# Optimization experiments

Hardware: AMD Instinct MI355X
Metric: run time of the kernel (lower is better)

The kernel has to match this reference:

```python
import jax, jax.numpy as jnp
import numpy as np

EMBED = 768
HEAD = 128

def setup_inputs() -> dict:
    key = jax.random.key(0)
    ks = jax.random.split(key, 8)
    B, S = 8, 2048
    x = jax.random.normal(ks[0], (B, S, EMBED), dtype=jnp.float32)
    enc_output = jax.random.normal(ks[1], (B, S, EMBED), dtype=jnp.float32)
    s = 1.0 / np.sqrt(EMBED)
    Wq = jax.random.normal(ks[2], (EMBED, HEAD), dtype=jnp.float32) * s
    Wk = jax.random.normal(ks[3], (EMBED, HEAD), dtype=jnp.float32) * s
    Wv = jax.random.normal(ks[4], (EMBED, HEAD), dtype=jnp.float32) * s
    bq = jnp.zeros((HEAD,), dtype=jnp.float32)
    bk = jnp.zeros((HEAD,), dtype=jnp.float32)
    bv = jnp.zeros((HEAD,), dtype=jnp.float32)
    return {"x": x, "enc_output": enc_output, "Wq": Wq, "bq": bq,
            "Wk": Wk, "bk": bk, "Wv": Wv, "bv": bv}

def reference(x, enc_output, Wq, bq, Wk, bk, Wv, bv):
    # Faithful to original: Q, K, V all from x (enc_output is unused in the
    # original forward); scale is embed_size ** 0.5; dropout never applied.
    q = jnp.einsum('nse,ed->nsd', x, Wq) + bq  # [B,S,H]
    k = jnp.einsum('nse,ed->nsd', x, Wk) + bk
    v = jnp.einsum('nse,ed->nsd', x, Wv) + bv
    energy = jnp.einsum('nqd,nkd->nqk', q, k)  # [B,S,S]
    attn = jax.nn.softmax(energy / jnp.sqrt(jnp.float32(EMBED)), axis=2)
    out = jnp.einsum('nql,nld->nqd', attn, v)  # [B,S,H]
    return out
```

## Files before the change

### kernel.cpp

```cpp
#include <hip/hip_runtime.h>
#include <hip/hip_bf16.h>


typedef __bf16 bf16x8 __attribute__((ext_vector_type(8)));
typedef float f32x4 __attribute__((ext_vector_type(4)));
using bf16 = __hip_bfloat16;

#define EMB 768
#define HD 128
#define SEQ 2048
#define BATCH 8
#define ROWS (BATCH * SEQ)
#define NSPLIT 4
#define TILES_PER_SPLIT (SEQ / 64 / NSPLIT)

__device__ inline void cvt_store8(bf16* dst, float4 a, float4 b) {
    union { bf16 h[8]; uint4 u; } t;
    t.h[0] = __float2bfloat16(a.x); t.h[1] = __float2bfloat16(a.y);
    t.h[2] = __float2bfloat16(a.z); t.h[3] = __float2bfloat16(a.w);
    t.h[4] = __float2bfloat16(b.x); t.h[5] = __float2bfloat16(b.y);
    t.h[6] = __float2bfloat16(b.z); t.h[7] = __float2bfloat16(b.w);
    *reinterpret_cast<uint4*>(dst) = t.u;
}

__global__ __launch_bounds__(256) void wt_kernel(
    const float* __restrict__ Wq, const float* __restrict__ Wk,
    const float* __restrict__ Wv, bf16* __restrict__ Wt)
{
    __shared__ float t_lds[32][33];
    const int tid = threadIdx.x;
    const int k0 = blockIdx.x * 32;
    const int n0 = blockIdx.y * 32;
    const int mtx = blockIdx.z;
    const float* W = (mtx == 0) ? Wq : (mtx == 1) ? Wk : Wv;
    const int j = tid & 31, i0 = tid >> 5;
#pragma unroll
    for (int c = 0; c < 4; ++c)
        t_lds[i0 + 8 * c][j] = W[(size_t)(k0 + i0 + 8 * c) * HD + n0 + j];
    __syncthreads();
#pragma unroll
    for (int c = 0; c < 4; ++c)
        Wt[(size_t)mtx * HD * EMB + (size_t)(n0 + i0 + 8 * c) * EMB + k0 + j] =
            __float2bfloat16(t_lds[j][i0 + 8 * c]);
}

__global__ __launch_bounds__(256) void qkv_kernel(
    const float* __restrict__ x, const bf16* __restrict__ Wt,
    const float* __restrict__ bq, const float* __restrict__ bk,
    const float* __restrict__ bv,
    bf16* __restrict__ Q, bf16* __restrict__ K, bf16* __restrict__ Vt)
{
    __shared__ alignas(16) bf16 a_lds[64][68];
    __shared__ alignas(16) bf16 b_lds[128][68];
    const int tid  = threadIdx.x;
    const int sel  = blockIdx.y;
    const int row0 = blockIdx.x * 64;
    const bf16* Wsel = Wt + (size_t)sel * HD * EMB;
    const int lane = tid & 63, wave = tid >> 6;
    const int lr = lane & 15, lq = lane >> 4;

    f32x4 acc[8];
#pragma unroll
    for (int j = 0; j < 8; ++j) acc[j] = f32x4{0.f, 0.f, 0.f, 0.f};

    for (int kt = 0; kt < EMB / 64; ++kt) {
#pragma unroll
        for (int c = 0; c < 2; ++c) {
            int lin = tid + c * 256;
            int r = lin >> 3, ch = lin & 7;
            const float* src = &x[(size_t)(row0 + r) * EMB + kt * 64 + ch * 8];
            float4 f0 = *reinterpret_cast<const float4*>(src);
            float4 f1 = *reinterpret_cast<const float4*>(src + 4);
            cvt_store8(&a_lds[r][ch * 8], f0, f1);
        }
#pragma unroll
        for (int c = 0; c < 4; ++c) {
            int lin = tid + c * 256;
            int r = lin >> 3, ch = lin & 7;
            *reinterpret_cast<uint4*>(&b_lds[r][ch * 8]) =
                *reinterpret_cast<const uint4*>(&Wsel[(size_t)r * EMB + kt * 64 + ch * 8]);
        }
        __syncthreads();
#pragma unroll
        for (int ks = 0; ks < 2; ++ks) {
            bf16x8 a = *reinterpret_cast<const bf16x8*>(&a_lds[wave * 16 + lr][ks * 32 + lq * 8]);
#pragma unroll
            for (int nt = 0; nt < 8; ++nt) {
                bf16x8 b = *reinterpret_cast<const bf16x8*>(&b_lds[nt * 16 + lr][ks * 32 + lq * 8]);
                acc[nt] = __builtin_amdgcn_mfma_f32_16x16x32_bf16(a, b, acc[nt], 0, 0, 0);
            }
        }
        __syncthreads();
    }

    bf16 (*o_lds)[132] = reinterpret_cast<bf16(*)[132]>(&b_lds[0][0]);
    const float* bias = (sel == 0) ? bq : (sel == 1) ? bk : bv;
#pragma unroll
    for (int nt = 0; nt < 8; ++nt) {
        int col = nt * 16 + lr;
        float bb = bias[col];
#pragma unroll
        for (int rg = 0; rg < 4; ++rg)
            o_lds[wave * 16 + lq * 4 + rg][col] = __float2bfloat16(acc[nt][rg] + bb);
    }
    __syncthreads();
    if (sel < 2) {
        bf16* dst = (sel == 0) ? Q : K;
#pragma unroll
        for (int c = 0; c < 4; ++c) {
            int lin = tid + c * 256;
            int r = lin >> 4, ch = lin & 15;
            *reinterpret_cast<uint4*>(&dst[(size_t)(row0 + r) * HD + ch * 8]) =
                *reinterpret_cast<const uint4*>(&o_lds[r][ch * 8]);
        }
    } else {
        int d = tid >> 1, sh = (tid & 1) * 32;
        int bi = row0 >> 11, s0 = row0 & (SEQ - 1);
        union { bf16 h[32]; uint4 u4[4]; } pk;
#pragma unroll
        for (int s = 0; s < 32; ++s) pk.h[s] = o_lds[sh + s][d];
        bf16* base = &Vt[((size_t)bi * HD + d) * SEQ + s0 + sh];
#pragma unroll
        for (int c = 0; c < 4; ++c)
            *reinterpret_cast<uint4*>(base + c * 8) = pk.u4[c];
    }
}

__global__ __launch_bounds__(256, 2) void flash_kernel(
    const bf16* __restrict__ Q, const bf16* __restrict__ K,
    const bf16* __restrict__ Vt,
    float* __restrict__ Opart, float* __restrict__ Lpart)
{
    __shared__ alignas(16) bf16 k_lds[64][132];
    __shared__ alignas(16) bf16 v_lds[144][68];
    __shared__ alignas(16) bf16 p_lds[4][32][72];
    const int tid = threadIdx.x;
    const int lane = tid & 63, wave = tid >> 6;
    const int lr = lane & 15, lq = lane >> 4;
    const int b  = blockIdx.y;
    const int split = blockIdx.z;
    const int q0 = blockIdx.x * 128;
    const int qrow = b * SEQ + q0 + wave * 32;

    const float sc = 0.03608439182435161f * 1.44269504088896f;

    for (int i = tid; i < 16 * 68; i += 256) {
        int r = i / 68, c = i % 68;
        v_lds[128 + r][c] = __float2bfloat16(r == 0 ? 1.0f : 0.0f);
    }

    bf16x8 qf[2][4];
#pragma unroll
    for (int qt = 0; qt < 2; ++qt)
#pragma unroll
        for (int ks = 0; ks < 4; ++ks)
            qf[qt][ks] = *reinterpret_cast<const bf16x8*>(
                &Q[(size_t)(qrow + qt * 16 + lr) * HD + ks * 32 + lq * 8]);

    f32x4 o[2][9];
#pragma unroll
    for (int qt = 0; qt < 2; ++qt)
#pragma unroll
        for (int d = 0; d < 9; ++d) o[qt][d] = f32x4{0.f, 0.f, 0.f, 0.f};

    for (int t = split * TILES_PER_SPLIT; t < (split + 1) * TILES_PER_SPLIT; ++t) {
        __syncthreads();
#pragma unroll
        for (int c = 0; c < 4; ++c) {
            int lin = tid + c * 256;
            int r = lin >> 4, ch = lin & 15;
            *reinterpret_cast<uint4*>(&k_lds[r][ch * 8]) =
                *reinterpret_cast<const uint4*>(&K[(size_t)(b * SEQ + t * 64 + r) * HD + ch * 8]);
        }
#pragma unroll
        for (int c = 0; c < 4; ++c) {
            int lin = tid + c * 256;
            int r = lin >> 3, ch = lin & 7;
            *reinterpret_cast<uint4*>(&v_lds[r][ch * 8]) =
                *reinterpret_cast<const uint4*>(&Vt[((size_t)b * HD + r) * SEQ + t * 64 + ch * 8]);
        }
        __syncthreads();

#pragma unroll
        for (int nt = 0; nt < 4; ++nt) {
            bf16x8 kf[4];
#pragma unroll
            for (int ks = 0; ks < 4; ++ks)
                kf[ks] = *reinterpret_cast<const bf16x8*>(&k_lds[nt * 16 + lr][ks * 32 + lq * 8]);
#pragma unroll
            for (int qt = 0; qt < 2; ++qt) {
                f32x4 s = f32x4{0.f, 0.f, 0.f, 0.f};
#pragma unroll
                for (int ks = 0; ks < 4; ++ks)
                    s = __builtin_amdgcn_mfma_f32_16x16x32_bf16(kf[ks], qf[qt][ks], s, 0, 0, 0);
                union { bf16 h[4]; uint2 u; } pk;
#pragma unroll
                for (int r = 0; r < 4; ++r)
                    pk.h[r] = __float2bfloat16(exp2f(__builtin_fmaf(s[r], sc, -8.0f)));
                *reinterpret_cast<uint2*>(&p_lds[wave][qt * 16 + lr][nt * 16 + lq * 4]) = pk.u;
            }
        }

#pragma unroll
        for (int ks = 0; ks < 2; ++ks) {
            bf16x8 pf[2];
#pragma unroll
            for (int qt = 0; qt < 2; ++qt)
                pf[qt] = *reinterpret_cast<const bf16x8*>(
                    &p_lds[wave][qt * 16 + lr][ks * 32 + lq * 8]);
#pragma unroll
            for (int d = 0; d < 9; ++d) {
                bf16x8 vf = *reinterpret_cast<const bf16x8*>(&v_lds[d * 16 + lr][ks * 32 + lq * 8]);
#pragma unroll
                for (int qt = 0; qt < 2; ++qt)
                    o[qt][d] = __builtin_amdgcn_mfma_f32_16x16x32_bf16(vf, pf[qt], o[qt][d], 0, 0, 0);
            }
        }
    }

    const size_t obase = (size_t)split * ROWS;
#pragma unroll
    for (int qt = 0; qt < 2; ++qt) {
#pragma unroll
        for (int d = 0; d < 8; ++d)
            *reinterpret_cast<f32x4*>(
                &Opart[(obase + qrow + qt * 16 + lr) * HD + d * 16 + lq * 4]) = o[qt][d];
        if (lane < 16)
            Lpart[obase + qrow + qt * 16 + lr] = o[qt][8][0];
    }
}

__global__ __launch_bounds__(256) void combine_kernel(
    const float* __restrict__ Opart, const float* __restrict__ Lpart,
    float* __restrict__ out)
{
    int gid = blockIdx.x * 256 + threadIdx.x;
    int row = gid >> 5, dc = gid & 31;
    float L = 0.f;
#pragma unroll
    for (int s = 0; s < NSPLIT; ++s)
        L += Lpart[(size_t)s * ROWS + row];
    float4 acc = {0.f, 0.f, 0.f, 0.f};
#pragma unroll
    for (int s = 0; s < NSPLIT; ++s) {
        float4 v = *reinterpret_cast<const float4*>(&Opart[((size_t)s * ROWS + row) * HD + dc * 4]);
        acc.x += v.x; acc.y += v.y; acc.z += v.z; acc.w += v.w;
    }
    float inv = 1.f / L;
    acc.x *= inv; acc.y *= inv; acc.z *= inv; acc.w *= inv;
    *reinterpret_cast<float4*>(&out[(size_t)row * HD + dc * 4]) = acc;
}

extern "C" void kernel_launch(void* const* d_in, const int* in_sizes, int n_in,
                              void* d_out, int out_size, void* d_ws, size_t ws_size,
                              hipStream_t stream) {
    const float* x  = (const float*)d_in[0];
    const float* Wq = (const float*)d_in[2];
    const float* bq = (const float*)d_in[3];
    const float* Wk = (const float*)d_in[4];
    const float* bk = (const float*)d_in[5];
    const float* Wv = (const float*)d_in[6];
    const float* bv = (const float*)d_in[7];
    float* out = (float*)d_out;

    char* ws = (char*)d_ws;
    const size_t WT_BYTES  = (size_t)3 * HD * EMB * 2;
    const size_t QKV_BYTES = (size_t)ROWS * HD * 2;
    const size_t OP_BYTES  = (size_t)NSPLIT * ROWS * HD * 4;
    bf16*  Wt    = (bf16*)ws;
    bf16*  Qb    = (bf16*)(ws + WT_BYTES);
    bf16*  Kb    = (bf16*)(ws + WT_BYTES + QKV_BYTES);
    bf16*  Vt    = (bf16*)(ws + WT_BYTES + 2 * QKV_BYTES);
    float* Opart = (float*)(ws + WT_BYTES + 3 * QKV_BYTES);
    float* Lpart = (float*)(ws + WT_BYTES + 3 * QKV_BYTES + OP_BYTES);

    hipLaunchKernelGGL(wt_kernel, dim3(EMB / 32, HD / 32, 3), dim3(256), 0, stream,
                       Wq, Wk, Wv, Wt);
    hipLaunchKernelGGL(qkv_kernel, dim3(ROWS / 64, 3), dim3(256), 0, stream,
                       x, Wt, bq, bk, bv, Qb, Kb, Vt);
    hipLaunchKernelGGL(flash_kernel, dim3(SEQ / 128, BATCH, NSPLIT), dim3(256), 0, stream,
                       Qb, Kb, Vt, Opart, Lpart);
    hipLaunchKernelGGL(combine_kernel, dim3(ROWS * 32 / 256), dim3(256), 0, stream,
                       Opart, Lpart, out);
}
```

Measured before the change: 193.7 us.

## Double-buffer weight tiles and load activations straight to MFMA registers in QKV

The QKV projection kernel now keeps B (weight) tiles in a double-buffered LDS ring with register prefetch two steps ahead. The activation A operand is read from global memory directly into the per-lane MFMA fragment layout, converted to bf16 in registers, and skips LDS. This drops one barrier per k-step and overlaps global loads with MFMA work. The cost is more register pressure, and the A reads per lane are less coalesced (16 rows per wave with strided access).

```diff
diff --git a/kernel.cpp b/kernel.cpp
--- a/kernel.cpp
+++ b/kernel.cpp
@@ -13,15 +13,6 @@
 #define ROWS (BATCH * SEQ)
 #define NSPLIT 4
 #define TILES_PER_SPLIT (SEQ / 64 / NSPLIT)
-
-__device__ inline void cvt_store8(bf16* dst, float4 a, float4 b) {
-    union { bf16 h[8]; uint4 u; } t;
-    t.h[0] = __float2bfloat16(a.x); t.h[1] = __float2bfloat16(a.y);
-    t.h[2] = __float2bfloat16(a.z); t.h[3] = __float2bfloat16(a.w);
-    t.h[4] = __float2bfloat16(b.x); t.h[5] = __float2bfloat16(b.y);
-    t.h[6] = __float2bfloat16(b.z); t.h[7] = __float2bfloat16(b.w);
-    *reinterpret_cast<uint4*>(dst) = t.u;
-}
 
 __global__ __launch_bounds__(256) void wt_kernel(
     const float* __restrict__ Wq, const float* __restrict__ Wk,
@@ -50,8 +41,7 @@
     const float* __restrict__ bv,
     bf16* __restrict__ Q, bf16* __restrict__ K, bf16* __restrict__ Vt)
 {
-    __shared__ alignas(16) bf16 a_lds[64][68];
-    __shared__ alignas(16) bf16 b_lds[128][68];
+    __shared__ alignas(16) bf16 b_lds[2][128][68];
     const int tid  = threadIdx.x;
     const int sel  = blockIdx.y;
     const int row0 = blockIdx.x * 64;
@@ -59,41 +49,77 @@
     const int lane = tid & 63, wave = tid >> 6;
     const int lr = lane & 15, lq = lane >> 4;
 
+    const float* arow = &x[(size_t)(row0 + wave * 16 + lr) * EMB + lq * 8];
+    const int br = tid >> 3, bch = tid & 7;
+
+    float4 araw[2][2];
+    uint4  braw[4];
+
+    auto loadA = [&](int kt) {
+#pragma unroll
+        for (int ks = 0; ks < 2; ++ks) {
+            const float* p = arow + kt * 64 + ks * 32;
+            araw[ks][0] = *reinterpret_cast<const float4*>(p);
+            araw[ks][1] = *reinterpret_cast<const float4*>(p + 4);
+        }
+    };
+    auto loadB = [&](int kt) {
+#pragma unroll
+        for (int c = 0; c < 4; ++c)
+            braw[c] = *reinterpret_cast<const uint4*>(
+                &Wsel[(size_t)(br + c * 32) * EMB + kt * 64 + bch * 8]);
+    };
+    auto writeB = [&](int pb) {
+#pragma unroll
+        for (int c = 0; c < 4; ++c)
+            *reinterpret_cast<uint4*>(&b_lds[pb][br + c * 32][bch * 8]) = braw[c];
+    };
+
     f32x4 acc[8];
 #pragma unroll
     for (int j = 0; j < 8; ++j) acc[j] = f32x4{0.f, 0.f, 0.f, 0.f};
 
+    loadA(0);
+    loadB(0);
+    writeB(0);
+    loadB(1);
+    asm volatile("s_waitcnt lgkmcnt(0)" ::: "memory");
+    __builtin_amdgcn_s_barrier();
+
     for (int kt = 0; kt < EMB / 64; ++kt) {
-#pragma unroll
-        for (int c = 0; c < 2; ++c) {
-            int lin = tid + c * 256;
-            int r = lin >> 3, ch = lin & 7;
-            const float* src = &x[(size_t)(row0 + r) * EMB + kt * 64 + ch * 8];
-            float4 f0 = *reinterpret_cast<const float4*>(src);
-            float4 f1 = *reinterpret_cast<const float4*>(src + 4);
-            cvt_store8(&a_lds[r][ch * 8], f0, f1);
-        }
-#pragma unroll
-        for (int c = 0; c < 4; ++c) {
-            int lin = tid + c * 256;
-            int r = lin >> 3, ch = lin & 7;
-            *reinterpret_cast<uint4*>(&b_lds[r][ch * 8]) =
-                *reinterpret_cast<const uint4*>(&Wsel[(size_t)r * EMB + kt * 64 + ch * 8]);
-        }
-        __syncthreads();
+        const int p = kt & 1;
+        bf16x8 af[2];
 #pragma unroll
         for (int ks = 0; ks < 2; ++ks) {
-            bf16x8 a = *reinterpret_cast<const bf16x8*>(&a_lds[wave * 16 + lr][ks * 32 + lq * 8]);
+            union { bf16 h[8]; bf16x8 v; } u;
+            u.h[0] = __float2bfloat16(araw[ks][0].x);
+            u.h[1] = __float2bfloat16(araw[ks][0].y);
+            u.h[2] = __float2bfloat16(araw[ks][0].z);
+            u.h[3] = __float2bfloat16(araw[ks][0].w);
+            u.h[4] = __float2bfloat16(araw[ks][1].x);
+            u.h[5] = __float2bfloat16(araw[ks][1].y);
+            u.h[6] = __float2bfloat16(araw[ks][1].z);
+            u.h[7] = __float2bfloat16(araw[ks][1].w);
+            af[ks] = u.v;
+        }
+        if (kt < 11) {
+            loadA(kt + 1);
+            writeB(p ^ 1);
+        }
+        if (kt < 10) loadB(kt + 2);
+#pragma unroll
+        for (int ks = 0; ks < 2; ++ks)
 #pragma unroll
             for (int nt = 0; nt < 8; ++nt) {
-                bf16x8 b = *reinterpret_cast<const bf16x8*>(&b_lds[nt * 16 + lr][ks * 32 + lq * 8]);
-                acc[nt] = __builtin_amdgcn_mfma_f32_16x16x32_bf16(a, b, acc[nt], 0, 0, 0);
+                bf16x8 b = *reinterpret_cast<const bf16x8*>(
+                    &b_lds[p][nt * 16 + lr][ks * 32 + lq * 8]);
+                acc[nt] = __builtin_amdgcn_mfma_f32_16x16x32_bf16(af[ks], b, acc[nt], 0, 0, 0);
             }
-        }
-        __syncthreads();
-    }
-
-    bf16 (*o_lds)[132] = reinterpret_cast<bf16(*)[132]>(&b_lds[0][0]);
+        asm volatile("s_waitcnt lgkmcnt(0)" ::: "memory");
+        __builtin_amdgcn_s_barrier();
+    }
+
+    bf16 (*o_lds)[132] = reinterpret_cast<bf16(*)[132]>(&b_lds[0][0][0]);
     const float* bias = (sel == 0) ? bq : (sel == 1) ? bk : bv;
 #pragma unroll
     for (int nt = 0; nt < 8; ++nt) {
```

After: 221.0 us. 1.14x slower.
